# Optimization experiments

Hardware: AMD Instinct MI355X
Metric: run time of the kernel (lower is better)

Reference implementation:

```python
import jax, jax.numpy as jnp
import numpy as np

N, E = 50000, 800000
F_IN, EDGE_DIM, H, C = 128, 64, 8, 32
NEG_SLOPE = 0.2


def setup_inputs() -> dict:
    key = jax.random.key(0)
    ks = jax.random.split(key, 9)
    return {
        "x": jax.random.normal(ks[0], (N, F_IN), dtype=jnp.float32),
        "edge_index": jax.random.randint(ks[1], (2, E), 0, N, dtype=jnp.int32),
        "edge_attr": jax.random.normal(ks[2], (E, EDGE_DIM), dtype=jnp.float32),
        "W": jax.random.normal(ks[3], (F_IN, H * C), dtype=jnp.float32) * 0.05,
        "att_src": jax.random.normal(ks[4], (H, C), dtype=jnp.float32) * 0.05,
        "att_dst": jax.random.normal(ks[5], (H, C), dtype=jnp.float32) * 0.05,
        "W_edge": jax.random.normal(ks[6], (EDGE_DIM, H * C), dtype=jnp.float32) * 0.05,
        "att_edge": jax.random.normal(ks[7], (H, C), dtype=jnp.float32) * 0.05,
        "bias": jax.random.normal(ks[8], (H * C,), dtype=jnp.float32) * 0.05,
    }


def reference(x, edge_index, edge_attr, W, att_src, att_dst, W_edge, att_edge, bias):
    src, dst = edge_index[0], edge_index[1]  # messages flow src -> dst
    # Pre-activation ReLU from Graph_intra.forward
    xr = jax.nn.relu(x)
    # Linear projection, per-head view: [N, H, C]
    xs = (xr @ W).reshape(N, H, C)
    # Per-node attention logits: [N, H]
    a_src = jnp.einsum("nhc,hc->nh", xs, att_src)
    a_dst = jnp.einsum("nhc,hc->nh", xs, att_dst)
    # Edge-feature attention contribution: [E, H]
    e_proj = (edge_attr @ W_edge).reshape(E, H, C)
    a_edge = jnp.einsum("ehc,hc->eh", e_proj, att_edge)
    # Per-edge logits + LeakyReLU
    alpha = jax.nn.leaky_relu(a_src[src] + a_dst[dst] + a_edge, NEG_SLOPE)  # [E, H]
    # Segment softmax over destination neighborhoods
    seg_max = jax.ops.segment_max(alpha, dst, num_segments=N)
    seg_max = jnp.where(jnp.isfinite(seg_max), seg_max, 0.0)
    alpha = jnp.exp(alpha - seg_max[dst])
    seg_sum = jax.ops.segment_sum(alpha, dst, num_segments=N)
    alpha = alpha / (seg_sum[dst] + 1e-16)
    # Weighted message aggregation: scatter-add alpha_e * x_src[e]
    msgs = alpha[:, :, None] * xs[src]  # [E, H, C]
    out = jax.ops.segment_sum(msgs, dst, num_segments=N)  # [N, H, C]
    return out.reshape(N, H * C) + bias
```

## Files before the change

kernel.cpp:

```cpp
#include <hip/hip_runtime.h>

#define N_NODES 50000
#define E_EDGES 800000
#define F_IN    128
#define EDGE_DIM 64
#define HC      256
#define NEG_SLOPE 0.2f

typedef __attribute__((ext_vector_type(8))) short short8;
typedef __attribute__((ext_vector_type(4))) float f32x4;

__device__ __forceinline__ unsigned short f2bf(float f) {
    unsigned u = __builtin_bit_cast(unsigned, f);
    u += 0x7fffu + ((u >> 16) & 1u);
    return (unsigned short)(u >> 16);
}
__device__ __forceinline__ float bf2f(unsigned short b) {
    return __builtin_bit_cast(float, (unsigned)b << 16);
}

__global__ __launch_bounds__(256) void k_pre(const float* __restrict__ W,
        const float* __restrict__ att_src, const float* __restrict__ att_dst,
        const float* __restrict__ W_edge, const float* __restrict__ att_edge,
        unsigned short* __restrict__ W_T, unsigned short* __restrict__ WaT,
        float* __restrict__ We_fold, int* __restrict__ counts, int* __restrict__ gcur) {
    int idx = blockIdx.x * 256 + threadIdx.x;
    if (idx < N_NODES) counts[idx] = 0;
    if (idx == 0) *gcur = 0;
    if (idx < 32768) {
        int n = idx >> 7, k = idx & 127;
        W_T[n * 128 + k] = f2bf(W[k * 256 + n]);
    }
    if (idx < 2048) {
        int col = idx & 15, k = idx >> 4;
        const float* att = (col < 8) ? att_src : att_dst;
        int h = col & 7;
        float s = 0.f;
        #pragma unroll
        for (int c = 0; c < 32; ++c)
            s = fmaf(W[k * 256 + h * 32 + c], att[h * 32 + c], s);
        WaT[col * 128 + k] = f2bf(s);
    }
    if (idx < 512) {
        int d = idx >> 3, h = idx & 7;
        float s = 0.f;
        #pragma unroll
        for (int c = 0; c < 32; ++c)
            s = fmaf(W_edge[d * 256 + h * 32 + c], att_edge[h * 32 + c], s);
        We_fold[d * 8 + h] = s;
    }
}

__global__ void k_hist(const int4* __restrict__ dst4, int* __restrict__ counts) {
    int i = blockIdx.x * 256 + threadIdx.x;
    if (i < E_EDGES / 4) {
        int4 d = dst4[i];
        atomicAdd(&counts[d.x], 1);
        atomicAdd(&counts[d.y], 1);
        atomicAdd(&counts[d.z], 1);
        atomicAdd(&counts[d.w], 1);
    }
}

#define NT_TILES 782
#define K1_GRID 512
__global__ __launch_bounds__(256, 2) void k1_mfma(const float* __restrict__ x,
        const unsigned short* __restrict__ W_T, const unsigned short* __restrict__ WaT,
        unsigned short* __restrict__ xs, float* __restrict__ a_src, float* __restrict__ a_dst) {
    __shared__ unsigned short sB[256 * 128];
    __shared__ unsigned short sA[64 * 128];
    int t = threadIdx.x;
    for (int G = t; G < 4096; G += 256) {
        int n = G >> 4, gi = G & 15;
        *(int4*)&sB[(n * 16 + (gi ^ (n & 7))) * 8] = *(const int4*)&W_T[n * 128 + gi * 8];
    }
    int lane = t & 63, w = t >> 6, mr = lane & 15, g = lane >> 4;
    short8 wa[4];
    #pragma unroll
    for (int ks = 0; ks < 4; ++ks)
        wa[ks] = *(const short8*)&WaT[mr * 128 + ks * 32 + g * 8];

    bool first = true;
    for (int rt = blockIdx.x; rt < NT_TILES; rt += K1_GRID) {
        if (!first) __syncthreads();
        first = false;
        for (int G = t; G < 1024; G += 256) {
            int r = G >> 4, gi = G & 15;
            int node = rt * 64 + r;
            unsigned short pk[8];
            if (node < N_NODES) {
                const float* xp = &x[(long)node * 128 + gi * 8];
                #pragma unroll
                for (int jj = 0; jj < 8; ++jj) pk[jj] = f2bf(fmaxf(xp[jj], 0.f));
            } else {
                #pragma unroll
                for (int jj = 0; jj < 8; ++jj) pk[jj] = 0;
            }
            *(int4*)&sA[(r * 16 + (gi ^ (r & 7))) * 8] = *(int4*)pk;
        }
        __syncthreads();

        f32x4 acc[17];
        #pragma unroll
        for (int i = 0; i < 17; ++i) acc[i] = (f32x4){0.f, 0.f, 0.f, 0.f};

        int r16 = w * 16 + mr;
        #pragma unroll
        for (int ks = 0; ks < 4; ++ks) {
            int pos = (ks * 4 + g) ^ (mr & 7);
            short8 a = *(const short8*)&sA[(r16 * 16 + pos) * 8];
            #pragma unroll
            for (int nt = 0; nt < 16; ++nt) {
                short8 b = *(const short8*)&sB[((nt * 16 + mr) * 16 + pos) * 8];
                acc[nt] = __builtin_amdgcn_mfma_f32_16x16x32_bf16(a, b, acc[nt], 0, 0, 0);
            }
            acc[16] = __builtin_amdgcn_mfma_f32_16x16x32_bf16(a, wa[ks], acc[16], 0, 0, 0);
        }

        #pragma unroll
        for (int r = 0; r < 4; ++r) {
            int node = rt * 64 + w * 16 + g * 4 + r;
            if (node < N_NODES) {
                #pragma unroll
                for (int nt = 0; nt < 16; ++nt)
                    xs[(long)node * 256 + nt * 16 + mr] = f2bf(acc[nt][r]);
                if (mr < 8) a_src[node * 8 + mr]       = acc[16][r];
                else        a_dst[node * 8 + (mr - 8)] = acc[16][r];
            }
        }
    }
}

__global__ __launch_bounds__(256) void k4_alloc(const int* __restrict__ counts,
                                                int* __restrict__ starts,
                                                int* __restrict__ cursor,
                                                int* __restrict__ gcur) {
    int n = blockIdx.x * 256 + threadIdx.x;
    int c = (n < N_NODES) ? counts[n] : 0;
    int incl = c;
    #pragma unroll
    for (int off = 1; off < 64; off <<= 1) {
        int u = __shfl_up(incl, off);
        if ((threadIdx.x & 63) >= off) incl += u;
    }
    int total = __shfl(incl, 63);
    int wavebase = 0;
    if ((threadIdx.x & 63) == 63) wavebase = atomicAdd(gcur, total);
    wavebase = __shfl(wavebase, 63);
    if (n < N_NODES) {
        int st = wavebase + incl - c;
        starts[n] = st;
        cursor[n] = st;
    }
}

__global__ __launch_bounds__(256) void k25_fused(const float4* __restrict__ edge_attr4,
        const float* __restrict__ We_fold,
        const int* __restrict__ src, const int* __restrict__ dst,
        const float* __restrict__ a_src, const float* __restrict__ a_dst,
        int* __restrict__ cursor,
        _Float16* __restrict__ w_perm, int* __restrict__ src_perm) {
    __shared__ __align__(16) float se[32 * 68];
    __shared__ __align__(16) float sfT[8 * 68];
    __shared__ int s_src[32], s_dst[32], s_pos[32];
    int t = threadIdx.x;
    long ebase = (long)blockIdx.x * 32;
    for (int i = t; i < 512; i += 256)
        sfT[(i & 7) * 68 + (i >> 3)] = We_fold[i];
    for (int i = t; i < 512; i += 256) {
        float4 v = edge_attr4[ebase * 16 + i];
        *(float4*)&se[(i >> 4) * 68 + (i & 15) * 4] = v;
    }
    if (t < 32) {
        int e = ebase + t;
        int d = dst[e];
        s_src[t] = src[e];
        s_dst[t] = d;
        s_pos[t] = atomicAdd(&cursor[d], 1);
    }
    __syncthreads();
    int e = t >> 3, h = t & 7;
    const float4* sa = (const float4*)&se[e * 68];
    const float4* sb = (const float4*)&sfT[h * 68];
    float s = 0.f;
    #pragma unroll
    for (int i = 0; i < 16; ++i) {
        float4 a = sa[i], b = sb[i];
        s = fmaf(a.x, b.x, s);
        s = fmaf(a.y, b.y, s);
        s = fmaf(a.z, b.z, s);
        s = fmaf(a.w, b.w, s);
    }
    int sn = s_src[e], dn = s_dst[e];
    float v = s + a_src[sn * 8 + h] + a_dst[dn * 8 + h];
    v = (v > 0.f) ? v : NEG_SLOPE * v;
    float w = __expf(v);
    int pos = s_pos[e];
    w_perm[(size_t)pos * 8 + h] = (_Float16)w;
    if (h == 0) src_perm[pos] = sn;
}

__global__ __launch_bounds__(256) void k6_wave(
    const int* __restrict__ starts, const int* __restrict__ counts,
    const _Float16* __restrict__ w_perm, const int* __restrict__ src_perm,
    const unsigned short* __restrict__ xs, const float* __restrict__ bias,
    float* __restrict__ out) {
    int lane = threadIdx.x & 63;
    int n = blockIdx.x * 4 + (threadIdx.x >> 6);
    if (n >= N_NODES) return;
    int start = starts[n], cnt = counts[n];
    int j = lane >> 3;
    int hq = lane >> 3;

    float acc0 = 0.f, acc1 = 0.f, acc2 = 0.f, acc3 = 0.f;
    float psum = 0.f;
    for (int base = 0; base < cnt; base += 8) {
        int nk = cnt - base; if (nk > 8) nk = 8;
        float wv = (float)w_perm[(size_t)(start + base) * 8 + lane];
        if (j >= nk) wv = 0.f;
        psum += wv;
        int sv = src_perm[start + base + (lane & 7)];
        #pragma unroll
        for (int jj = 0; jj < 8; ++jj) {
            int s = __shfl(sv, jj);
            s = (jj < nk) ? s : 0;
            float w = __shfl(wv, jj * 8 + hq);
            ushort4 xv = *(const ushort4*)&xs[(size_t)s * 256 + lane * 4];
            acc0 = fmaf(w, bf2f(xv.x), acc0);
            acc1 = fmaf(w, bf2f(xv.y), acc1);
            acc2 = fmaf(w, bf2f(xv.z), acc2);
            acc3 = fmaf(w, bf2f(xv.w), acc3);
        }
    }
    psum += __shfl_xor(psum, 8);
    psum += __shfl_xor(psum, 16);
    psum += __shfl_xor(psum, 32);
    float denom = __shfl(psum, hq);
    float rinv = 1.0f / (denom + 1e-16f);
    float4 bv = *(const float4*)&bias[lane * 4];
    float4 o;
    o.x = acc0 * rinv + bv.x;
    o.y = acc1 * rinv + bv.y;
    o.z = acc2 * rinv + bv.z;
    o.w = acc3 * rinv + bv.w;
    *(float4*)&out[(size_t)n * 256 + lane * 4] = o;
}

extern "C" void kernel_launch(void* const* d_in, const int* in_sizes, int n_in,
                              void* d_out, int out_size, void* d_ws, size_t ws_size,
                              hipStream_t stream) {
    const float* x         = (const float*)d_in[0];
    const int*   ei        = (const int*)d_in[1];
    const float* edge_attr = (const float*)d_in[2];
    const float* W         = (const float*)d_in[3];
    const float* att_src   = (const float*)d_in[4];
    const float* att_dst   = (const float*)d_in[5];
    const float* W_edge    = (const float*)d_in[6];
    const float* att_edge  = (const float*)d_in[7];
    const float* bias      = (const float*)d_in[8];
    float* out = (float*)d_out;

    const int* e_src = ei;
    const int* e_dst = ei + E_EDGES;

    char* p = (char*)d_ws;
    unsigned short* xs = (unsigned short*)p; p += (size_t)N_NODES * HC * 2;
    float* a_src   = (float*)p; p += (size_t)N_NODES * 8 * 4;
    float* a_dst   = (float*)p; p += (size_t)N_NODES * 8 * 4;
    _Float16* w_perm = (_Float16*)p; p += (size_t)E_EDGES * 8 * 2 + 256;
    int* src_perm  = (int*)p;   p += (size_t)E_EDGES * 4 + 256;
    unsigned short* W_T  = (unsigned short*)p; p += 32768 * 2;
    unsigned short* WaT  = (unsigned short*)p; p += 2048 * 2;
    float* We_fold = (float*)p; p += 512 * 4;
    int* counts    = (int*)p;   p += 200192;
    int* starts    = (int*)p;   p += 200192;
    int* cursor    = (int*)p;   p += 200192;
    int* gcur      = (int*)p;   p += 256;

    hipLaunchKernelGGL(k_pre, dim3(196), dim3(256), 0, stream,
                       W, att_src, att_dst, W_edge, att_edge, W_T, WaT, We_fold, counts, gcur);
    hipLaunchKernelGGL(k_hist, dim3((E_EDGES / 4 + 255) / 256), dim3(256), 0, stream,
                       (const int4*)e_dst, counts);
    hipLaunchKernelGGL(k1_mfma, dim3(K1_GRID), dim3(256), 0, stream,
                       x, W_T, WaT, xs, a_src, a_dst);
    hipLaunchKernelGGL(k4_alloc, dim3(196), dim3(256), 0, stream,
                       counts, starts, cursor, gcur);
    hipLaunchKernelGGL(k25_fused, dim3(E_EDGES / 32), dim3(256), 0, stream,
                       (const float4*)edge_attr, We_fold, e_src, e_dst,
                       a_src, a_dst, cursor, w_perm, src_perm);
    hipLaunchKernelGGL(k6_wave, dim3(N_NODES / 4), dim3(256), 0, stream,
                       starts, counts, w_perm, src_perm, xs, bias, out);
}
```

Measured before the change: 222.7 us.

## Fuse histogram into projection kernel, batch edge tiles, use nontemporal stores

Merges the destination-degree histogram kernel into the MFMA projection kernel as extra blocks, removing one launch and letting the atomics overlap with the GEMM. The edge-logit kernel now loops over 8 tiles of 32 edges per block, so the folded edge weights are loaded once per block rather than once per tile. Nontemporal loads and stores are added for the permuted weight and source arrays and for the output. The trade-offs are a smaller edge grid with extra syncs per block, and the GEMM blocks now dispatch after the histogram blocks.

New measurement: 222.8 us. Within noise of the previous version (+0.0%).

```diff
diff --git a/kernel.cpp b/kernel.cpp
--- a/kernel.cpp
+++ b/kernel.cpp
@@ -51,25 +51,30 @@
     }
 }
 
-__global__ void k_hist(const int4* __restrict__ dst4, int* __restrict__ counts) {
-    int i = blockIdx.x * 256 + threadIdx.x;
-    if (i < E_EDGES / 4) {
-        int4 d = dst4[i];
-        atomicAdd(&counts[d.x], 1);
-        atomicAdd(&counts[d.y], 1);
-        atomicAdd(&counts[d.z], 1);
-        atomicAdd(&counts[d.w], 1);
-    }
-}
-
 #define NT_TILES 782
 #define K1_GRID 512
-__global__ __launch_bounds__(256, 2) void k1_mfma(const float* __restrict__ x,
+#define HIST_BLOCKS 782
+__global__ __launch_bounds__(256, 2) void k1h(const float* __restrict__ x,
         const unsigned short* __restrict__ W_T, const unsigned short* __restrict__ WaT,
+        const int4* __restrict__ dst4, int* __restrict__ counts,
         unsigned short* __restrict__ xs, float* __restrict__ a_src, float* __restrict__ a_dst) {
     __shared__ unsigned short sB[256 * 128];
     __shared__ unsigned short sA[64 * 128];
     int t = threadIdx.x;
+
+    if (blockIdx.x < HIST_BLOCKS) {
+        int i = blockIdx.x * 256 + t;
+        if (i < E_EDGES / 4) {
+            int4 d = dst4[i];
+            atomicAdd(&counts[d.x], 1);
+            atomicAdd(&counts[d.y], 1);
+            atomicAdd(&counts[d.z], 1);
+            atomicAdd(&counts[d.w], 1);
+        }
+        return;
+    }
+    int bid = blockIdx.x - HIST_BLOCKS;
+
     for (int G = t; G < 4096; G += 256) {
         int n = G >> 4, gi = G & 15;
         *(int4*)&sB[(n * 16 + (gi ^ (n & 7))) * 8] = *(const int4*)&W_T[n * 128 + gi * 8];
@@ -81,7 +86,7 @@
         wa[ks] = *(const short8*)&WaT[mr * 128 + ks * 32 + g * 8];
 
     bool first = true;
-    for (int rt = blockIdx.x; rt < NT_TILES; rt += K1_GRID) {
+    for (int rt = bid; rt < NT_TILES; rt += K1_GRID) {
         if (!first) __syncthreads();
         first = false;
         for (int G = t; G < 1024; G += 256) {
@@ -154,6 +159,7 @@
     }
 }
 
+#define K25_TILES 8
 __global__ __launch_bounds__(256) void k25_fused(const float4* __restrict__ edge_attr4,
         const float* __restrict__ We_fold,
         const int* __restrict__ src, const int* __restrict__ dst,
@@ -164,40 +170,46 @@
     __shared__ __align__(16) float sfT[8 * 68];
     __shared__ int s_src[32], s_dst[32], s_pos[32];
     int t = threadIdx.x;
-    long ebase = (long)blockIdx.x * 32;
     for (int i = t; i < 512; i += 256)
         sfT[(i & 7) * 68 + (i >> 3)] = We_fold[i];
-    for (int i = t; i < 512; i += 256) {
-        float4 v = edge_attr4[ebase * 16 + i];
-        *(float4*)&se[(i >> 4) * 68 + (i & 15) * 4] = v;
-    }
-    if (t < 32) {
-        int e = ebase + t;
-        int d = dst[e];
-        s_src[t] = src[e];
-        s_dst[t] = d;
-        s_pos[t] = atomicAdd(&cursor[d], 1);
-    }
-    __syncthreads();
+
     int e = t >> 3, h = t & 7;
-    const float4* sa = (const float4*)&se[e * 68];
-    const float4* sb = (const float4*)&sfT[h * 68];
-    float s = 0.f;
-    #pragma unroll
-    for (int i = 0; i < 16; ++i) {
-        float4 a = sa[i], b = sb[i];
-        s = fmaf(a.x, b.x, s);
-        s = fmaf(a.y, b.y, s);
-        s = fmaf(a.z, b.z, s);
-        s = fmaf(a.w, b.w, s);
-    }
-    int sn = s_src[e], dn = s_dst[e];
-    float v = s + a_src[sn * 8 + h] + a_dst[dn * 8 + h];
-    v = (v > 0.f) ? v : NEG_SLOPE * v;
-    float w = __expf(v);
-    int pos = s_pos[e];
-    w_perm[(size_t)pos * 8 + h] = (_Float16)w;
-    if (h == 0) src_perm[pos] = sn;
+    #pragma unroll 1
+    for (int it = 0; it < K25_TILES; ++it) {
+        long ebase = (long)blockIdx.x * (32 * K25_TILES) + it * 32;
+        __syncthreads();
+        for (int i = t; i < 512; i += 256) {
+            float4 v = edge_attr4[ebase * 16 + i];
+            *(float4*)&se[(i >> 4) * 68 + (i & 15) * 4] = v;
+        }
+        if (t < 32) {
+            int ee = ebase + t;
+            int d = dst[ee];
+            s_src[t] = src[ee];
+            s_dst[t] = d;
+            s_pos[t] = atomicAdd(&cursor[d], 1);
+        }
+        __syncthreads();
+
+        const float4* sa = (const float4*)&se[e * 68];
+        const float4* sb = (const float4*)&sfT[h * 68];
+        float s = 0.f;
+        #pragma unroll
+        for (int i = 0; i < 16; ++i) {
+            float4 a = sa[i], b = sb[i];
+            s = fmaf(a.x, b.x, s);
+            s = fmaf(a.y, b.y, s);
+            s = fmaf(a.z, b.z, s);
+            s = fmaf(a.w, b.w, s);
+        }
+        int sn = s_src[e], dn = s_dst[e];
+        float v = s + a_src[sn * 8 + h] + a_dst[dn * 8 + h];
+        v = (v > 0.f) ? v : NEG_SLOPE * v;
+        float w = __expf(v);
+        int pos = s_pos[e];
+        __builtin_nontemporal_store((_Float16)w, &w_perm[(size_t)pos * 8 + h]);
+        if (h == 0) __builtin_nontemporal_store(sn, &src_perm[pos]);
+    }
 }
 
 __global__ __launch_bounds__(256) void k6_wave(
@@ -216,10 +228,10 @@
     float psum = 0.f;
     for (int base = 0; base < cnt; base += 8) {
         int nk = cnt - base; if (nk > 8) nk = 8;
-        float wv = (float)w_perm[(size_t)(start + base) * 8 + lane];
+        float wv = (float)__builtin_nontemporal_load(&w_perm[(size_t)(start + base) * 8 + lane]);
         if (j >= nk) wv = 0.f;
         psum += wv;
-        int sv = src_perm[start + base + (lane & 7)];
+        int sv = __builtin_nontemporal_load(&src_perm[start + base + (lane & 7)]);
         #pragma unroll
         for (int jj = 0; jj < 8; ++jj) {
             int s = __shfl(sv, jj);
@@ -238,12 +250,12 @@
     float denom = __shfl(psum, hq);
     float rinv = 1.0f / (denom + 1e-16f);
     float4 bv = *(const float4*)&bias[lane * 4];
-    float4 o;
-    o.x = acc0 * rinv + bv.x;
-    o.y = acc1 * rinv + bv.y;
-    o.z = acc2 * rinv + bv.z;
-    o.w = acc3 * rinv + bv.w;
-    *(float4*)&out[(size_t)n * 256 + lane * 4] = o;
+    f32x4 o;
+    o[0] = acc0 * rinv + bv.x;
+    o[1] = acc1 * rinv + bv.y;
+    o[2] = acc2 * rinv + bv.z;
+    o[3] = acc3 * rinv + bv.w;
+    __builtin_nontemporal_store(o, (f32x4*)&out[(size_t)n * 256 + lane * 4]);
 }
 
 extern "C" void kernel_launch(void* const* d_in, const int* in_sizes, int n_in,
@@ -279,13 +291,11 @@
 
     hipLaunchKernelGGL(k_pre, dim3(196), dim3(256), 0, stream,
                        W, att_src, att_dst, W_edge, att_edge, W_T, WaT, We_fold, counts, gcur);
-    hipLaunchKernelGGL(k_hist, dim3((E_EDGES / 4 + 255) / 256), dim3(256), 0, stream,
-                       (const int4*)e_dst, counts);
-    hipLaunchKernelGGL(k1_mfma, dim3(K1_GRID), dim3(256), 0, stream,
-                       x, W_T, WaT, xs, a_src, a_dst);
+    hipLaunchKernelGGL(k1h, dim3(HIST_BLOCKS + K1_GRID), dim3(256), 0, stream,
+                       x, W_T, WaT, (const int4*)e_dst, counts, xs, a_src, a_dst);
     hipLaunchKernelGGL(k4_alloc, dim3(196), dim3(256), 0, stream,
                        counts, starts, cursor, gcur);
-    hipLaunchKernelGGL(k25_fused, dim3(E_EDGES / 32), dim3(256), 0, stream,
+    hipLaunchKernelGGL(k25_fused, dim3(E_EDGES / (32 * K25_TILES)), dim3(256), 0, stream,
                        (const float4*)edge_attr, We_fold, e_src, e_dst,
                        a_src, a_dst, cursor, w_perm, src_perm);
     hipLaunchKernelGGL(k6_wave, dim3(N_NODES / 4), dim3(256), 0, stream,
```
